# Optimization experiments

Measured on AMD Instinct MI355X. Metric: run time of the kernel, lower is better.

## Reference

```python
import jax, jax.numpy as jnp
import numpy as np

B, HID = 32768, 128
NU = 0.49                 # poisson_ratio default
LAM_PHYS, LAM_EL = 0.1, 0.05
EPS = 1e-7


def setup_inputs() -> dict:
    key = jax.random.key(0)
    ks = jax.random.split(key, 8)
    def w(k, shape, fan_in):
        return jax.random.normal(k, shape, jnp.float32) / np.float32(np.sqrt(fan_in))
    return {
        "coords": jax.random.normal(ks[0], (B, 3), jnp.float32),
        "target_labels": jax.random.uniform(ks[1], (B, 1), jnp.float32),
        "target_stiffness": jax.random.uniform(ks[2], (B, 1), jnp.float32) * 10.0,
        "W1": w(ks[3], (3, HID), 3), "b1": jnp.zeros((HID,), jnp.float32),
        "W2": w(ks[4], (HID, HID), HID), "b2": jnp.zeros((HID,), jnp.float32),
        "Wp": w(ks[5], (HID, 1), HID), "bp": jnp.zeros((1,), jnp.float32),
        "Ws": w(ks[6], (HID, 1), HID), "bs": jnp.zeros((1,), jnp.float32),
        "Wd": w(ks[7], (HID, 3), HID), "bd": jnp.zeros((3,), jnp.float32),
    }


def reference(coords, target_labels, target_stiffness,
              W1, b1, W2, b2, Wp, bp, Ws, bs, Wd, bd):
    def feats(x):  # x: (...,3) -> (...,HID)
        h = jnp.tanh(x @ W1 + b1)
        return jnp.tanh(h @ W2 + b2)

    h = feats(coords)                                   # (B,HID)
    prediction = jax.nn.sigmoid(h @ Wp + bp)            # (B,1)
    stiffness = jax.nn.softplus(h @ Ws + bs)            # (B,1) Young's modulus E

    # displacement field u(x): R^3 -> R^3, pointwise
    def disp_fn(x):  # (3,) -> (3,)
        return feats(x) @ Wd + bd

    # Per-point Hessian H[b,i,j,k] = d2 u_i / dx_j dx_k  (B,3,3,3)
    Hm = jax.vmap(jax.jacfwd(jax.jacfwd(disp_fn)))(coords)
    laplacian = jnp.einsum('bijj->bi', Hm)              # (B,3) lap(u_i)
    grad_div = jnp.einsum('biik->bk', Hm)               # (B,3) grad(div u)

    # Lame parameters from E (matches torch code incl. nu_denom clamp)
    mu = stiffness / (2.0 * (1.0 + NU))
    nu_denom = max(1.0 - 2.0 * NU, 1e-5)
    lmbda = stiffness * NU / ((1.0 + NU) * nu_denom)
    residual = mu * laplacian + (lmbda + mu) * grad_div  # (B,3)
    phys_loss = jnp.mean(jnp.sum(residual ** 2, axis=-1))

    # BCE on clamped prediction/labels
    p = jnp.clip(prediction, EPS, 1.0 - EPS)
    t = jnp.clip(target_labels, 0.0, 1.0)
    bce = -jnp.mean(t * jnp.log(p) + (1.0 - t) * jnp.log(1.0 - p))
    data_loss = bce + 0.5 * jnp.mean((stiffness - target_stiffness) ** 2)

    elastic_loss = jnp.mean(jax.nn.relu(-stiffness) + jax.nn.relu(stiffness - 15.0))

    total = data_loss + LAM_PHYS * phys_loss + LAM_EL * elastic_loss
    raw_losses = jnp.stack([data_loss, phys_loss, elastic_loss])
    return total, raw_losses
```

## Files before the change

### kernel.cpp

```cpp
#include <hip/hip_runtime.h>
#include <math.h>

#define HIDN 128
#define NPTS 32768
#define PTS_PER_BLK 16
#define NBLK (NPTS / PTS_PER_BLK)

#define MU_COEF 0.33557046979865773f
#define LM_COEF 16.442953020134228f

typedef float f32x4  __attribute__((ext_vector_type(4)));
typedef short bf16x8 __attribute__((ext_vector_type(8)));


__device__ __forceinline__ unsigned short f2bf(float f) {
    unsigned u = __builtin_bit_cast(unsigned, f);
    u += 0x7fffu + ((u >> 16) & 1u);
    return (unsigned short)(u >> 16);
}

__device__ __forceinline__ float tanh_fast(float x) {
    float e = __builtin_amdgcn_exp2f(x * 2.885390081777927f);
    return 1.0f - 2.0f * __builtin_amdgcn_rcpf(e + 1.0f);
}

__global__ void prep_kernel(const float* __restrict__ W1,
                            const float* __restrict__ b1,
                            const float* __restrict__ W2,
                            float* __restrict__ ws)
{
    float* accum = ws;
    float* tab   = ws + 128;
    unsigned short* W2bf = (unsigned short*)(ws + 2048);
    int tid = blockIdx.x * blockDim.x + threadIdx.x;
    if (tid < 8) accum[tid] = 0.0f;
    if (tid < HIDN) {
        float w0 = W1[0 * HIDN + tid];
        float w1 = W1[1 * HIDN + tid];
        float w2 = W1[2 * HIDN + tid];
        float* t = tab + tid * 12;
        t[0] = w0; t[1] = w1; t[2] = w2; t[3] = b1[tid];
        t[4] = w0 * w0; t[5] = w0 * w1; t[6] = w0 * w2;
        t[7] = w1 * w1; t[8] = w1 * w2; t[9] = w2 * w2;
        t[10] = 0.0f; t[11] = 0.0f;
    }
    for (int i = tid; i < HIDN * HIDN; i += gridDim.x * blockDim.x) {
        int m = i >> 7, h = i & 127;
        W2bf[m * HIDN + h] = f2bf(W2[h * HIDN + m]);
    }
}

__global__ __launch_bounds__(256, 3) void pinn_main(
    const float* __restrict__ coords,
    const float* __restrict__ labels,
    const float* __restrict__ tstiff,
    const float* __restrict__ b2,
    const float* __restrict__ Wp, const float* __restrict__ bp,
    const float* __restrict__ Wsv, const float* __restrict__ bs,
    const float* __restrict__ Wd,
    const float* __restrict__ ws_ro,
    float* __restrict__ accum)
{
    const float* tab = ws_ro + 128;
    const unsigned short* W2bf = (const unsigned short*)(ws_ro + 2048);

    __shared__ __align__(16) char smem[43584];
    unsigned short* A  = (unsigned short*)smem;
    float*          red  = (float*)smem;
    float*          red2 = (float*)(smem + 43520);

    const int tid  = threadIdx.x;
    const int wave = __builtin_amdgcn_readfirstlane(tid >> 6);
    const int lane = tid & 63;
    const int blk  = blockIdx.x;

    {
        const int b  = tid & 15;
        const int hc = tid >> 4;
        const int h0 = hc * 8;
        const int gb = blk * PTS_PER_BLK + b;
        const float x0 = coords[gb * 3 + 0];
        const float x1 = coords[gb * 3 + 1];
        const float x2 = coords[gb * 3 + 2];
        unsigned pk[10][4];
#pragma unroll
        for (int i = 0; i < 8; ++i) {
            const float* t = tab + (h0 + i) * 12;
            float z = fmaf(x0, t[0], fmaf(x1, t[1], fmaf(x2, t[2], t[3])));
            float a  = tanh_fast(z);
            float g  = fmaf(-a, a, 1.0f);
            float ag = a * g;
            float c[10];
            c[0] = a;
            c[1] = g * t[0]; c[2] = g * t[1]; c[3] = g * t[2];
            c[4] = ag * t[4]; c[5] = ag * t[5]; c[6] = ag * t[6];
            c[7] = ag * t[7]; c[8] = ag * t[8]; c[9] = ag * t[9];
#pragma unroll
            for (int ch = 0; ch < 10; ++ch) {
                unsigned v = f2bf(c[ch]);
                if ((i & 1) == 0) pk[ch][i >> 1] = v;
                else              pk[ch][i >> 1] |= v << 16;
            }
        }
#pragma unroll
        for (int ch = 0; ch < 10; ++ch) {
            uint4* dst = (uint4*)(A + ch * (16 * 136) + b * 136 + h0);
            *dst = make_uint4(pk[ch][0], pk[ch][1], pk[ch][2], pk[ch][3]);
        }
    }
    __syncthreads();

    const int l = lane & 15;
    const int q = lane >> 4;

    f32x4 acc[10][2] = {};
#pragma unroll
    for (int ks = 0; ks < 4; ++ks) {
        const int hk = ks * 32 + q * 8;
        bf16x8 bfr[2];
#pragma unroll
        for (int mt = 0; mt < 2; ++mt) {
            const int m = wave * 32 + mt * 16 + l;
            bfr[mt] = *(const bf16x8*)(W2bf + m * HIDN + hk);
        }
#pragma unroll
        for (int ch = 0; ch < 10; ++ch) {
            bf16x8 afr = *(const bf16x8*)(A + ch * (16 * 136) + l * 136 + hk);
            acc[ch][0] = __builtin_amdgcn_mfma_f32_16x16x32_bf16(afr, bfr[0], acc[ch][0], 0, 0, 0);
            acc[ch][1] = __builtin_amdgcn_mfma_f32_16x16x32_bf16(afr, bfr[1], acc[ch][1], 0, 0, 0);
        }
    }

    float sum[4][8] = {};
#pragma unroll
    for (int mt = 0; mt < 2; ++mt) {
        const int m = wave * 32 + mt * 16 + l;
        const float wd0 = Wd[m * 3 + 0];
        const float wd1 = Wd[m * 3 + 1];
        const float wd2 = Wd[m * 3 + 2];
        const float wp  = Wp[m];
        const float wsv = Wsv[m];
        const float b2v = b2[m];
#pragma unroll
        for (int r = 0; r < 4; ++r) {
            const float z2 = acc[0][mt][r] + b2v;
            const float a2 = tanh_fast(z2);
            const float g2 = fmaf(-a2, a2, 1.0f);
            const float d2 = -2.0f * a2 * g2;
            const float t0 = acc[1][mt][r], t1 = acc[2][mt][r], t2 = acc[3][mt][r];
            const float q00 = acc[4][mt][r], q01 = acc[5][mt][r], q02 = acc[6][mt][r];
            const float q11 = acc[7][mt][r], q12 = acc[8][mt][r], q22 = acc[9][mt][r];
            const float qtr = q00 + q11 + q22;
            const float tt  = t0 * t0 + t1 * t1 + t2 * t2;
            const float Lm  = fmaf(-2.0f * g2, qtr, d2 * tt);
            const float wt  = wd0 * t0 + wd1 * t1 + wd2 * t2;
            const float m2g2 = -2.0f * g2;
            const float dwt  = d2 * wt;
            const float r0 = wd0 * q00 + wd1 * q01 + wd2 * q02;
            const float r1 = wd0 * q01 + wd1 * q11 + wd2 * q12;
            const float r2 = wd0 * q02 + wd1 * q12 + wd2 * q22;
            sum[r][0] += wp  * a2;
            sum[r][1] += wsv * a2;
            sum[r][2] += wd0 * Lm;
            sum[r][3] += wd1 * Lm;
            sum[r][4] += wd2 * Lm;
            sum[r][5] += m2g2 * r0 + dwt * t0;
            sum[r][6] += m2g2 * r1 + dwt * t1;
            sum[r][7] += m2g2 * r2 + dwt * t2;
        }
    }
    __syncthreads();

#pragma unroll
    for (int r = 0; r < 4; ++r) {
        const int b = q * 4 + r;
        const int slot = wave * 16 + l;
        float4* dst = (float4*)(red + (b * 64 + slot) * 8);
        dst[0] = make_float4(sum[r][0], sum[r][1], sum[r][2], sum[r][3]);
        dst[1] = make_float4(sum[r][4], sum[r][5], sum[r][6], sum[r][7]);
    }
    __syncthreads();

    {
        const int b  = tid >> 4;
        const int l2 = tid & 15;
        float v[8] = {};
#pragma unroll
        for (int w = 0; w < 4; ++w) {
            const float4* src = (const float4*)(red + (b * 64 + w * 16 + l2) * 8);
            float4 p0 = src[0], p1 = src[1];
            v[0] += p0.x; v[1] += p0.y; v[2] += p0.z; v[3] += p0.w;
            v[4] += p1.x; v[5] += p1.y; v[6] += p1.z; v[7] += p1.w;
        }
#pragma unroll
        for (int k = 0; k < 8; ++k) {
            v[k] += __shfl_xor(v[k], 1);
            v[k] += __shfl_xor(v[k], 2);
            v[k] += __shfl_xor(v[k], 4);
            v[k] += __shfl_xor(v[k], 8);
        }
        float bce_t = 0.f, sq_t = 0.f, phys_t = 0.f, el_t = 0.f;
        if (l2 == 0) {
            const int gb = blk * PTS_PER_BLK + b;
            const float fzp = v[0] + bp[0];
            const float fzs = v[1] + bs[0];
            float pred = 1.0f / (1.0f + expf(-fzp));
            pred = fminf(fmaxf(pred, 1e-7f), 1.0f - 1e-7f);
            const float E = fmaxf(fzs, 0.0f) + log1pf(expf(-fabsf(fzs)));
            const float mu = E * MU_COEF;
            const float cc = E * LM_COEF + mu;
            const float rr0 = mu * v[2] + cc * v[5];
            const float rr1 = mu * v[3] + cc * v[6];
            const float rr2 = mu * v[4] + cc * v[7];
            phys_t = rr0 * rr0 + rr1 * rr1 + rr2 * rr2;
            float tl = labels[gb];
            tl = fminf(fmaxf(tl, 0.0f), 1.0f);
            bce_t = -(tl * logf(pred) + (1.0f - tl) * logf(1.0f - pred));
            const float dsv = E - tstiff[gb];
            sq_t = dsv * dsv;
            el_t = fmaxf(-E, 0.0f) + fmaxf(E - 15.0f, 0.0f);
        }
#pragma unroll
        for (int m = 16; m < 64; m <<= 1) {
            bce_t  += __shfl_xor(bce_t, m);
            sq_t   += __shfl_xor(sq_t, m);
            phys_t += __shfl_xor(phys_t, m);
            el_t   += __shfl_xor(el_t, m);
        }
        if (lane == 0) {
            red2[wave * 4 + 0] = bce_t;
            red2[wave * 4 + 1] = sq_t;
            red2[wave * 4 + 2] = phys_t;
            red2[wave * 4 + 3] = el_t;
        }
    }
    __syncthreads();
    if (tid < 4) {
        float s = red2[0 * 4 + tid] + red2[1 * 4 + tid] + red2[2 * 4 + tid] + red2[3 * 4 + tid];
        atomicAdd(accum + tid, s);
    }
}

__global__ void finalize_kernel(const float* __restrict__ accum,
                                float* __restrict__ out)
{
    if (threadIdx.x == 0 && blockIdx.x == 0) {
        const float invB = 1.0f / (float)NPTS;
        const float bce  = accum[0] * invB;
        const float data = bce + 0.5f * accum[1] * invB;
        const float phys = accum[2] * invB;
        const float el   = accum[3] * invB;
        out[0] = data + 0.1f * phys + 0.05f * el;
        out[1] = data;
        out[2] = phys;
        out[3] = el;
    }
}

extern "C" void kernel_launch(void* const* d_in, const int* in_sizes, int n_in,
                              void* d_out, int out_size, void* d_ws, size_t ws_size,
                              hipStream_t stream)
{
    const float* coords = (const float*)d_in[0];
    const float* labels = (const float*)d_in[1];
    const float* tstiff = (const float*)d_in[2];
    const float* W1  = (const float*)d_in[3];
    const float* b1  = (const float*)d_in[4];
    const float* W2  = (const float*)d_in[5];
    const float* b2  = (const float*)d_in[6];
    const float* Wp  = (const float*)d_in[7];
    const float* bp  = (const float*)d_in[8];
    const float* Wsv = (const float*)d_in[9];
    const float* bs  = (const float*)d_in[10];
    const float* Wd  = (const float*)d_in[11];

    float* ws  = (float*)d_ws;
    float* out = (float*)d_out;

    prep_kernel<<<64, 256, 0, stream>>>(W1, b1, W2, ws);
    pinn_main<<<NBLK, 256, 0, stream>>>(coords, labels, tstiff, b2,
                                        Wp, bp, Wsv, bs, Wd, ws, ws);
    finalize_kernel<<<1, 64, 0, stream>>>(ws, out);
}
```

Measured before the change: 116.4 us.

## Swizzle LDS layout, swap MFMA operands, and simplify per-block reduction

The first-layer features now go into a row-major LDS tile with an XOR swizzle instead of padded rows, and W1/b1 are read with vector loads in place of a precomputed table. Packing uses the hardware v_cvt_pk_bf16_f32 instruction. The MFMA operands are swapped so each lane's accumulators belong to a single point, which lets the per-point reduction use cross-lane shuffles plus one small LDS pass and drops one barrier. Per-hidden-unit output weights are packed into a vectorized table. The changes target LDS bank conflicts, conversion cost and reduction overhead, at the price of depending on inline asm and a swizzle indexing scheme.

```diff
diff --git a/kernel.cpp b/kernel.cpp
--- a/kernel.cpp
+++ b/kernel.cpp
@@ -12,41 +12,42 @@
 typedef float f32x4  __attribute__((ext_vector_type(4)));
 typedef short bf16x8 __attribute__((ext_vector_type(8)));
 
-
 __device__ __forceinline__ unsigned short f2bf(float f) {
     unsigned u = __builtin_bit_cast(unsigned, f);
     u += 0x7fffu + ((u >> 16) & 1u);
     return (unsigned short)(u >> 16);
 }
 
+__device__ __forceinline__ unsigned cvtpk2(float lo, float hi) {
+    unsigned r;
+    asm("v_cvt_pk_bf16_f32 %0, %1, %2" : "=v"(r) : "v"(lo), "v"(hi));
+    return r;
+}
+
 __device__ __forceinline__ float tanh_fast(float x) {
     float e = __builtin_amdgcn_exp2f(x * 2.885390081777927f);
     return 1.0f - 2.0f * __builtin_amdgcn_rcpf(e + 1.0f);
 }
 
-__global__ void prep_kernel(const float* __restrict__ W1,
-                            const float* __restrict__ b1,
-                            const float* __restrict__ W2,
+__global__ void prep_kernel(const float* __restrict__ W2,
+                            const float* __restrict__ Wd,
+                            const float* __restrict__ Wp,
+                            const float* __restrict__ Wsv,
+                            const float* __restrict__ b2,
                             float* __restrict__ ws)
 {
-    float* accum = ws;
-    float* tab   = ws + 128;
+    int tid = blockIdx.x * blockDim.x + threadIdx.x;
+    if (tid < 8) ws[tid] = 0.0f;
+    if (tid < HIDN) {
+        float* mt = ws + 64 + tid * 8;
+        mt[0] = Wd[tid * 3 + 0]; mt[1] = Wd[tid * 3 + 1]; mt[2] = Wd[tid * 3 + 2];
+        mt[3] = Wp[tid]; mt[4] = Wsv[tid]; mt[5] = b2[tid];
+        mt[6] = 0.0f; mt[7] = 0.0f;
+    }
     unsigned short* W2bf = (unsigned short*)(ws + 2048);
-    int tid = blockIdx.x * blockDim.x + threadIdx.x;
-    if (tid < 8) accum[tid] = 0.0f;
-    if (tid < HIDN) {
-        float w0 = W1[0 * HIDN + tid];
-        float w1 = W1[1 * HIDN + tid];
-        float w2 = W1[2 * HIDN + tid];
-        float* t = tab + tid * 12;
-        t[0] = w0; t[1] = w1; t[2] = w2; t[3] = b1[tid];
-        t[4] = w0 * w0; t[5] = w0 * w1; t[6] = w0 * w2;
-        t[7] = w1 * w1; t[8] = w1 * w2; t[9] = w2 * w2;
-        t[10] = 0.0f; t[11] = 0.0f;
-    }
     for (int i = tid; i < HIDN * HIDN; i += gridDim.x * blockDim.x) {
-        int m = i >> 7, h = i & 127;
-        W2bf[m * HIDN + h] = f2bf(W2[h * HIDN + m]);
+        int h = i >> 7, m = i & 127;
+        W2bf[m * HIDN + h] = f2bf(W2[i]);
     }
 }
 
@@ -54,20 +55,18 @@
     const float* __restrict__ coords,
     const float* __restrict__ labels,
     const float* __restrict__ tstiff,
-    const float* __restrict__ b2,
-    const float* __restrict__ Wp, const float* __restrict__ bp,
-    const float* __restrict__ Wsv, const float* __restrict__ bs,
-    const float* __restrict__ Wd,
+    const float* __restrict__ W1,
+    const float* __restrict__ b1,
+    const float* __restrict__ bp,
+    const float* __restrict__ bs,
     const float* __restrict__ ws_ro,
     float* __restrict__ accum)
 {
-    const float* tab = ws_ro + 128;
+    const float* mtab = ws_ro + 64;
     const unsigned short* W2bf = (const unsigned short*)(ws_ro + 2048);
 
-    __shared__ __align__(16) char smem[43584];
-    unsigned short* A  = (unsigned short*)smem;
-    float*          red  = (float*)smem;
-    float*          red2 = (float*)(smem + 43520);
+    __shared__ __align__(16) char smem[43008];
+    float* red2 = (float*)(smem + 40960);
 
     const int tid  = threadIdx.x;
     const int wave = __builtin_amdgcn_readfirstlane(tid >> 6);
@@ -75,74 +74,85 @@
     const int blk  = blockIdx.x;
 
     {
-        const int b  = tid & 15;
-        const int hc = tid >> 4;
+        const int b  = tid >> 4;
+        const int hc = tid & 15;
         const int h0 = hc * 8;
         const int gb = blk * PTS_PER_BLK + b;
         const float x0 = coords[gb * 3 + 0];
         const float x1 = coords[gb * 3 + 1];
         const float x2 = coords[gb * 3 + 2];
+        const f32x4 w0lo = *(const f32x4*)(W1 + h0);
+        const f32x4 w0hi = *(const f32x4*)(W1 + h0 + 4);
+        const f32x4 w1lo = *(const f32x4*)(W1 + HIDN + h0);
+        const f32x4 w1hi = *(const f32x4*)(W1 + HIDN + h0 + 4);
+        const f32x4 w2lo = *(const f32x4*)(W1 + 2 * HIDN + h0);
+        const f32x4 w2hi = *(const f32x4*)(W1 + 2 * HIDN + h0 + 4);
+        const f32x4 blo  = *(const f32x4*)(b1 + h0);
+        const f32x4 bhi  = *(const f32x4*)(b1 + h0 + 4);
+
         unsigned pk[10][4];
 #pragma unroll
-        for (int i = 0; i < 8; ++i) {
-            const float* t = tab + (h0 + i) * 12;
-            float z = fmaf(x0, t[0], fmaf(x1, t[1], fmaf(x2, t[2], t[3])));
-            float a  = tanh_fast(z);
-            float g  = fmaf(-a, a, 1.0f);
-            float ag = a * g;
-            float c[10];
-            c[0] = a;
-            c[1] = g * t[0]; c[2] = g * t[1]; c[3] = g * t[2];
-            c[4] = ag * t[4]; c[5] = ag * t[5]; c[6] = ag * t[6];
-            c[7] = ag * t[7]; c[8] = ag * t[8]; c[9] = ag * t[9];
-#pragma unroll
-            for (int ch = 0; ch < 10; ++ch) {
-                unsigned v = f2bf(c[ch]);
-                if ((i & 1) == 0) pk[ch][i >> 1] = v;
-                else              pk[ch][i >> 1] |= v << 16;
+        for (int p = 0; p < 4; ++p) {
+            float ca[2][10];
+#pragma unroll
+            for (int s = 0; s < 2; ++s) {
+                const int i = 2 * p + s;
+                const float wa = (i < 4) ? w0lo[i & 3] : w0hi[i & 3];
+                const float wb = (i < 4) ? w1lo[i & 3] : w1hi[i & 3];
+                const float wc = (i < 4) ? w2lo[i & 3] : w2hi[i & 3];
+                const float bb = (i < 4) ? blo[i & 3]  : bhi[i & 3];
+                const float z  = fmaf(x0, wa, fmaf(x1, wb, fmaf(x2, wc, bb)));
+                const float a  = tanh_fast(z);
+                const float g  = fmaf(-a, a, 1.0f);
+                const float ag = a * g;
+                const float p0 = ag * wa, p1 = ag * wb, p2 = ag * wc;
+                ca[s][0] = a;
+                ca[s][1] = g * wa; ca[s][2] = g * wb; ca[s][3] = g * wc;
+                ca[s][4] = p0 * wa; ca[s][5] = p0 * wb; ca[s][6] = p0 * wc;
+                ca[s][7] = p1 * wb; ca[s][8] = p1 * wc; ca[s][9] = p2 * wc;
             }
-        }
+#pragma unroll
+            for (int ch = 0; ch < 10; ++ch)
+                pk[ch][p] = cvtpk2(ca[0][ch], ca[1][ch]);
+        }
+        const int sw = (h0 * 2) ^ ((b & 7) << 4);
 #pragma unroll
         for (int ch = 0; ch < 10; ++ch) {
-            uint4* dst = (uint4*)(A + ch * (16 * 136) + b * 136 + h0);
-            *dst = make_uint4(pk[ch][0], pk[ch][1], pk[ch][2], pk[ch][3]);
+            *(uint4*)(smem + ch * 4096 + b * 256 + sw) =
+                make_uint4(pk[ch][0], pk[ch][1], pk[ch][2], pk[ch][3]);
         }
     }
     __syncthreads();
 
     const int l = lane & 15;
     const int q = lane >> 4;
+    const int lsw = (l & 7) << 4;
 
     f32x4 acc[10][2] = {};
 #pragma unroll
     for (int ks = 0; ks < 4; ++ks) {
         const int hk = ks * 32 + q * 8;
-        bf16x8 bfr[2];
-#pragma unroll
-        for (int mt = 0; mt < 2; ++mt) {
-            const int m = wave * 32 + mt * 16 + l;
-            bfr[mt] = *(const bf16x8*)(W2bf + m * HIDN + hk);
-        }
+        bf16x8 bfr0 = *(const bf16x8*)(W2bf + (wave * 32 + l) * HIDN + hk);
+        bf16x8 bfr1 = *(const bf16x8*)(W2bf + (wave * 32 + 16 + l) * HIDN + hk);
+        const int coff = (ks * 64 + q * 16) ^ lsw;
 #pragma unroll
         for (int ch = 0; ch < 10; ++ch) {
-            bf16x8 afr = *(const bf16x8*)(A + ch * (16 * 136) + l * 136 + hk);
-            acc[ch][0] = __builtin_amdgcn_mfma_f32_16x16x32_bf16(afr, bfr[0], acc[ch][0], 0, 0, 0);
-            acc[ch][1] = __builtin_amdgcn_mfma_f32_16x16x32_bf16(afr, bfr[1], acc[ch][1], 0, 0, 0);
-        }
-    }
-
-    float sum[4][8] = {};
+            bf16x8 afr = *(const bf16x8*)(smem + ch * 4096 + l * 256 + coff);
+            acc[ch][0] = __builtin_amdgcn_mfma_f32_16x16x32_bf16(bfr0, afr, acc[ch][0], 0, 0, 0);
+            acc[ch][1] = __builtin_amdgcn_mfma_f32_16x16x32_bf16(bfr1, afr, acc[ch][1], 0, 0, 0);
+        }
+    }
+
+    float sum[8] = {0, 0, 0, 0, 0, 0, 0, 0};
 #pragma unroll
     for (int mt = 0; mt < 2; ++mt) {
-        const int m = wave * 32 + mt * 16 + l;
-        const float wd0 = Wd[m * 3 + 0];
-        const float wd1 = Wd[m * 3 + 1];
-        const float wd2 = Wd[m * 3 + 2];
-        const float wp  = Wp[m];
-        const float wsv = Wsv[m];
-        const float b2v = b2[m];
 #pragma unroll
         for (int r = 0; r < 4; ++r) {
+            const int m = wave * 32 + mt * 16 + q * 4 + r;
+            const f32x4 mw0 = *(const f32x4*)(mtab + m * 8);
+            const f32x4 mw1 = *(const f32x4*)(mtab + m * 8 + 4);
+            const float wd0 = mw0[0], wd1 = mw0[1], wd2 = mw0[2], wpv = mw0[3];
+            const float wsv = mw1[0], b2v = mw1[1];
             const float z2 = acc[0][mt][r] + b2v;
             const float a2 = tanh_fast(z2);
             const float g2 = fmaf(-a2, a2, 1.0f);
@@ -152,92 +162,76 @@
             const float q11 = acc[7][mt][r], q12 = acc[8][mt][r], q22 = acc[9][mt][r];
             const float qtr = q00 + q11 + q22;
             const float tt  = t0 * t0 + t1 * t1 + t2 * t2;
-            const float Lm  = fmaf(-2.0f * g2, qtr, d2 * tt);
+            const float m2g2 = -2.0f * g2;
+            const float Lm  = fmaf(m2g2, qtr, d2 * tt);
             const float wt  = wd0 * t0 + wd1 * t1 + wd2 * t2;
-            const float m2g2 = -2.0f * g2;
-            const float dwt  = d2 * wt;
+            const float dwt = d2 * wt;
             const float r0 = wd0 * q00 + wd1 * q01 + wd2 * q02;
             const float r1 = wd0 * q01 + wd1 * q11 + wd2 * q12;
             const float r2 = wd0 * q02 + wd1 * q12 + wd2 * q22;
-            sum[r][0] += wp  * a2;
-            sum[r][1] += wsv * a2;
-            sum[r][2] += wd0 * Lm;
-            sum[r][3] += wd1 * Lm;
-            sum[r][4] += wd2 * Lm;
-            sum[r][5] += m2g2 * r0 + dwt * t0;
-            sum[r][6] += m2g2 * r1 + dwt * t1;
-            sum[r][7] += m2g2 * r2 + dwt * t2;
-        }
+            sum[0] = fmaf(wpv, a2, sum[0]);
+            sum[1] = fmaf(wsv, a2, sum[1]);
+            sum[2] = fmaf(wd0, Lm, sum[2]);
+            sum[3] = fmaf(wd1, Lm, sum[3]);
+            sum[4] = fmaf(wd2, Lm, sum[4]);
+            sum[5] += fmaf(m2g2, r0, dwt * t0);
+            sum[6] += fmaf(m2g2, r1, dwt * t1);
+            sum[7] += fmaf(m2g2, r2, dwt * t2);
+        }
+    }
+
+#pragma unroll
+    for (int k = 0; k < 8; ++k) {
+        sum[k] += __shfl_xor(sum[k], 16);
+        sum[k] += __shfl_xor(sum[k], 32);
+    }
+    if (q == 0) {
+        float4* dst = (float4*)(red2 + (wave * 16 + l) * 8);
+        dst[0] = make_float4(sum[0], sum[1], sum[2], sum[3]);
+        dst[1] = make_float4(sum[4], sum[5], sum[6], sum[7]);
     }
     __syncthreads();
 
-#pragma unroll
-    for (int r = 0; r < 4; ++r) {
-        const int b = q * 4 + r;
-        const int slot = wave * 16 + l;
-        float4* dst = (float4*)(red + (b * 64 + slot) * 8);
-        dst[0] = make_float4(sum[r][0], sum[r][1], sum[r][2], sum[r][3]);
-        dst[1] = make_float4(sum[r][4], sum[r][5], sum[r][6], sum[r][7]);
-    }
-    __syncthreads();
-
-    {
-        const int b  = tid >> 4;
-        const int l2 = tid & 15;
-        float v[8] = {};
+    if (tid < 16) {
+        float v[8] = {0, 0, 0, 0, 0, 0, 0, 0};
 #pragma unroll
         for (int w = 0; w < 4; ++w) {
-            const float4* src = (const float4*)(red + (b * 64 + w * 16 + l2) * 8);
-            float4 p0 = src[0], p1 = src[1];
-            v[0] += p0.x; v[1] += p0.y; v[2] += p0.z; v[3] += p0.w;
-            v[4] += p1.x; v[5] += p1.y; v[6] += p1.z; v[7] += p1.w;
-        }
-#pragma unroll
-        for (int k = 0; k < 8; ++k) {
-            v[k] += __shfl_xor(v[k], 1);
-            v[k] += __shfl_xor(v[k], 2);
-            v[k] += __shfl_xor(v[k], 4);
-            v[k] += __shfl_xor(v[k], 8);
-        }
-        float bce_t = 0.f, sq_t = 0.f, phys_t = 0.f, el_t = 0.f;
-        if (l2 == 0) {
-            const int gb = blk * PTS_PER_BLK + b;
-            const float fzp = v[0] + bp[0];
-            const float fzs = v[1] + bs[0];
-            float pred = 1.0f / (1.0f + expf(-fzp));
-            pred = fminf(fmaxf(pred, 1e-7f), 1.0f - 1e-7f);
-            const float E = fmaxf(fzs, 0.0f) + log1pf(expf(-fabsf(fzs)));
-            const float mu = E * MU_COEF;
-            const float cc = E * LM_COEF + mu;
-            const float rr0 = mu * v[2] + cc * v[5];
-            const float rr1 = mu * v[3] + cc * v[6];
-            const float rr2 = mu * v[4] + cc * v[7];
-            phys_t = rr0 * rr0 + rr1 * rr1 + rr2 * rr2;
-            float tl = labels[gb];
-            tl = fminf(fmaxf(tl, 0.0f), 1.0f);
-            bce_t = -(tl * logf(pred) + (1.0f - tl) * logf(1.0f - pred));
-            const float dsv = E - tstiff[gb];
-            sq_t = dsv * dsv;
-            el_t = fmaxf(-E, 0.0f) + fmaxf(E - 15.0f, 0.0f);
-        }
-#pragma unroll
-        for (int m = 16; m < 64; m <<= 1) {
-            bce_t  += __shfl_xor(bce_t, m);
-            sq_t   += __shfl_xor(sq_t, m);
-            phys_t += __shfl_xor(phys_t, m);
-            el_t   += __shfl_xor(el_t, m);
-        }
-        if (lane == 0) {
-            red2[wave * 4 + 0] = bce_t;
-            red2[wave * 4 + 1] = sq_t;
-            red2[wave * 4 + 2] = phys_t;
-            red2[wave * 4 + 3] = el_t;
-        }
-    }
-    __syncthreads();
-    if (tid < 4) {
-        float s = red2[0 * 4 + tid] + red2[1 * 4 + tid] + red2[2 * 4 + tid] + red2[3 * 4 + tid];
-        atomicAdd(accum + tid, s);
+            const float4* s = (const float4*)(red2 + (w * 16 + tid) * 8);
+            const float4 pa = s[0], pb = s[1];
+            v[0] += pa.x; v[1] += pa.y; v[2] += pa.z; v[3] += pa.w;
+            v[4] += pb.x; v[5] += pb.y; v[6] += pb.z; v[7] += pb.w;
+        }
+        const int gb = blk * PTS_PER_BLK + tid;
+        const float fzp = v[0] + bp[0];
+        const float fzs = v[1] + bs[0];
+        float pred = 1.0f / (1.0f + expf(-fzp));
+        pred = fminf(fmaxf(pred, 1e-7f), 1.0f - 1e-7f);
+        const float E = fmaxf(fzs, 0.0f) + log1pf(expf(-fabsf(fzs)));
+        const float mu = E * MU_COEF;
+        const float cc = E * LM_COEF + mu;
+        const float rr0 = mu * v[2] + cc * v[5];
+        const float rr1 = mu * v[3] + cc * v[6];
+        const float rr2 = mu * v[4] + cc * v[7];
+        float phys_t = rr0 * rr0 + rr1 * rr1 + rr2 * rr2;
+        float tl = labels[gb];
+        tl = fminf(fmaxf(tl, 0.0f), 1.0f);
+        float bce_t = -(tl * logf(pred) + (1.0f - tl) * logf(1.0f - pred));
+        const float dsv = E - tstiff[gb];
+        float sq_t = dsv * dsv;
+        float el_t = fmaxf(-E, 0.0f) + fmaxf(E - 15.0f, 0.0f);
+#pragma unroll
+        for (int mk = 1; mk < 16; mk <<= 1) {
+            bce_t  += __shfl_xor(bce_t, mk);
+            sq_t   += __shfl_xor(sq_t, mk);
+            phys_t += __shfl_xor(phys_t, mk);
+            el_t   += __shfl_xor(el_t, mk);
+        }
+        if (tid == 0) {
+            atomicAdd(accum + 0, bce_t);
+            atomicAdd(accum + 1, sq_t);
+            atomicAdd(accum + 2, phys_t);
+            atomicAdd(accum + 3, el_t);
+        }
     }
 }
 
@@ -277,8 +271,8 @@
     float* ws  = (float*)d_ws;
     float* out = (float*)d_out;
 
-    prep_kernel<<<64, 256, 0, stream>>>(W1, b1, W2, ws);
-    pinn_main<<<NBLK, 256, 0, stream>>>(coords, labels, tstiff, b2,
-                                        Wp, bp, Wsv, bs, Wd, ws, ws);
+    prep_kernel<<<64, 256, 0, stream>>>(W2, Wd, Wp, Wsv, b2, ws);
+    pinn_main<<<NBLK, 256, 0, stream>>>(coords, labels, tstiff, W1, b1,
+                                        bp, bs, ws, ws);
     finalize_kernel<<<1, 64, 0, stream>>>(ws, out);
 }
```

Result: slower. 192.4 us (+65.3%).

## Split pinn_main work across 8 waves per block with 512 threads

Applied to the files above, without the earlier changes.

Doubles the block to 512 threads so each thread builds 4 hidden units of the layer-1 tables and each wave owns one 16-column MFMA tile instead of two. This halves per-thread accumulators and registers and raises the launch-bounds occupancy target, so more waves can hide latency. The cross-wave reduction gains a shuffle step that folds column pairs before the shared-memory stage, keeping the same 64-slot layout. The cost is more waves per block, each with less independent work, and B-fragment loads from W2bf that are no longer shared across two tiles.

```diff
diff --git a/kernel.cpp b/kernel.cpp
--- a/kernel.cpp
+++ b/kernel.cpp
@@ -50,7 +50,7 @@
     }
 }
 
-__global__ __launch_bounds__(256, 3) void pinn_main(
+__global__ __launch_bounds__(512, 4) void pinn_main(
     const float* __restrict__ coords,
     const float* __restrict__ labels,
     const float* __restrict__ tstiff,
@@ -76,15 +76,15 @@
 
     {
         const int b  = tid & 15;
-        const int hc = tid >> 4;
-        const int h0 = hc * 8;
+        const int hb = tid >> 4;
+        const int h0 = hb * 4;
         const int gb = blk * PTS_PER_BLK + b;
         const float x0 = coords[gb * 3 + 0];
         const float x1 = coords[gb * 3 + 1];
         const float x2 = coords[gb * 3 + 2];
-        unsigned pk[10][4];
-#pragma unroll
-        for (int i = 0; i < 8; ++i) {
+        unsigned pk[10][2];
+#pragma unroll
+        for (int i = 0; i < 4; ++i) {
             const float* t = tab + (h0 + i) * 12;
             float z = fmaf(x0, t[0], fmaf(x1, t[1], fmaf(x2, t[2], t[3])));
             float a  = tanh_fast(z);
@@ -104,8 +104,8 @@
         }
 #pragma unroll
         for (int ch = 0; ch < 10; ++ch) {
-            uint4* dst = (uint4*)(A + ch * (16 * 136) + b * 136 + h0);
-            *dst = make_uint4(pk[ch][0], pk[ch][1], pk[ch][2], pk[ch][3]);
+            uint2* dst = (uint2*)(A + ch * (16 * 136) + b * 136 + h0);
+            *dst = make_uint2(pk[ch][0], pk[ch][1]);
         }
     }
     __syncthreads();
@@ -113,28 +113,22 @@
     const int l = lane & 15;
     const int q = lane >> 4;
 
-    f32x4 acc[10][2] = {};
+    f32x4 acc[10] = {};
 #pragma unroll
     for (int ks = 0; ks < 4; ++ks) {
         const int hk = ks * 32 + q * 8;
-        bf16x8 bfr[2];
-#pragma unroll
-        for (int mt = 0; mt < 2; ++mt) {
-            const int m = wave * 32 + mt * 16 + l;
-            bfr[mt] = *(const bf16x8*)(W2bf + m * HIDN + hk);
-        }
+        const int m = wave * 16 + l;
+        bf16x8 bfr = *(const bf16x8*)(W2bf + m * HIDN + hk);
 #pragma unroll
         for (int ch = 0; ch < 10; ++ch) {
             bf16x8 afr = *(const bf16x8*)(A + ch * (16 * 136) + l * 136 + hk);
-            acc[ch][0] = __builtin_amdgcn_mfma_f32_16x16x32_bf16(afr, bfr[0], acc[ch][0], 0, 0, 0);
-            acc[ch][1] = __builtin_amdgcn_mfma_f32_16x16x32_bf16(afr, bfr[1], acc[ch][1], 0, 0, 0);
+            acc[ch] = __builtin_amdgcn_mfma_f32_16x16x32_bf16(afr, bfr, acc[ch], 0, 0, 0);
         }
     }
 
     float sum[4][8] = {};
-#pragma unroll
-    for (int mt = 0; mt < 2; ++mt) {
-        const int m = wave * 32 + mt * 16 + l;
+    {
+        const int m = wave * 16 + l;
         const float wd0 = Wd[m * 3 + 0];
         const float wd1 = Wd[m * 3 + 1];
         const float wd2 = Wd[m * 3 + 2];
@@ -143,13 +137,13 @@
         const float b2v = b2[m];
 #pragma unroll
         for (int r = 0; r < 4; ++r) {
-            const float z2 = acc[0][mt][r] + b2v;
+            const float z2 = acc[0][r] + b2v;
             const float a2 = tanh_fast(z2);
             const float g2 = fmaf(-a2, a2, 1.0f);
             const float d2 = -2.0f * a2 * g2;
-            const float t0 = acc[1][mt][r], t1 = acc[2][mt][r], t2 = acc[3][mt][r];
-            const float q00 = acc[4][mt][r], q01 = acc[5][mt][r], q02 = acc[6][mt][r];
-            const float q11 = acc[7][mt][r], q12 = acc[8][mt][r], q22 = acc[9][mt][r];
+            const float t0 = acc[1][r], t1 = acc[2][r], t2 = acc[3][r];
+            const float q00 = acc[4][r], q01 = acc[5][r], q02 = acc[6][r];
+            const float q11 = acc[7][r], q12 = acc[8][r], q22 = acc[9][r];
             const float qtr = q00 + q11 + q22;
             const float tt  = t0 * t0 + t1 * t1 + t2 * t2;
             const float Lm  = fmaf(-2.0f * g2, qtr, d2 * tt);
@@ -169,19 +163,28 @@
             sum[r][7] += m2g2 * r2 + dwt * t2;
         }
     }
-    __syncthreads();
-
-#pragma unroll
-    for (int r = 0; r < 4; ++r) {
-        const int b = q * 4 + r;
-        const int slot = wave * 16 + l;
-        float4* dst = (float4*)(red + (b * 64 + slot) * 8);
-        dst[0] = make_float4(sum[r][0], sum[r][1], sum[r][2], sum[r][3]);
-        dst[1] = make_float4(sum[r][4], sum[r][5], sum[r][6], sum[r][7]);
-    }
-    __syncthreads();
-
-    {
+
+#pragma unroll
+    for (int r = 0; r < 4; ++r)
+#pragma unroll
+        for (int k = 0; k < 8; ++k)
+            sum[r][k] += __shfl_xor(sum[r][k], 8);
+
+    __syncthreads();
+
+    if (l < 8) {
+#pragma unroll
+        for (int r = 0; r < 4; ++r) {
+            const int b = q * 4 + r;
+            const int slot = wave * 8 + l;
+            float4* dst = (float4*)(red + (b * 64 + slot) * 8);
+            dst[0] = make_float4(sum[r][0], sum[r][1], sum[r][2], sum[r][3]);
+            dst[1] = make_float4(sum[r][4], sum[r][5], sum[r][6], sum[r][7]);
+        }
+    }
+    __syncthreads();
+
+    if (tid < 256) {
         const int b  = tid >> 4;
         const int l2 = tid & 15;
         float v[8] = {};
@@ -221,11 +224,11 @@
             el_t = fmaxf(-E, 0.0f) + fmaxf(E - 15.0f, 0.0f);
         }
 #pragma unroll
-        for (int m = 16; m < 64; m <<= 1) {
-            bce_t  += __shfl_xor(bce_t, m);
-            sq_t   += __shfl_xor(sq_t, m);
-            phys_t += __shfl_xor(phys_t, m);
-            el_t   += __shfl_xor(el_t, m);
+        for (int mk = 16; mk < 64; mk <<= 1) {
+            bce_t  += __shfl_xor(bce_t, mk);
+            sq_t   += __shfl_xor(sq_t, mk);
+            phys_t += __shfl_xor(phys_t, mk);
+            el_t   += __shfl_xor(el_t, mk);
         }
         if (lane == 0) {
             red2[wave * 4 + 0] = bce_t;
@@ -278,7 +281,7 @@
     float* out = (float*)d_out;
 
     prep_kernel<<<64, 256, 0, stream>>>(W1, b1, W2, ws);
-    pinn_main<<<NBLK, 256, 0, stream>>>(coords, labels, tstiff, b2,
+    pinn_main<<<NBLK, 512, 0, stream>>>(coords, labels, tstiff, b2,
                                         Wp, bp, Wsv, bs, Wd, ws, ws);
     finalize_kernel<<<1, 64, 0, stream>>>(ws, out);
 }
```

After: 117.9 us. No clear change (+1.3%).

## Process four point tiles per block, keeping W2 fragments in registers

Applied to the files above, without the earlier changes.

Each block now loops over four 16-point tiles instead of one, and the grid shrinks by the same factor. The W2 bf16 B-fragments and the per-column epilogue weights are loaded into registers once and reused for every tile. Loss partials are accumulated across tiles before a single atomic per block. This cuts redundant global weight loads and atomics, but it adds extra barriers per tile, raises register pressure (launch bounds lowered from 3 to 2 blocks per CU), and leaves fewer blocks to hide latency.

```diff
diff --git a/kernel.cpp b/kernel.cpp
--- a/kernel.cpp
+++ b/kernel.cpp
@@ -4,7 +4,8 @@
 #define HIDN 128
 #define NPTS 32768
 #define PTS_PER_BLK 16
-#define NBLK (NPTS / PTS_PER_BLK)
+#define TILES 4
+#define NBLK (NPTS / PTS_PER_BLK / TILES)
 
 #define MU_COEF 0.33557046979865773f
 #define LM_COEF 16.442953020134228f
@@ -50,7 +51,7 @@
     }
 }
 
-__global__ __launch_bounds__(256, 3) void pinn_main(
+__global__ __launch_bounds__(256, 2) void pinn_main(
     const float* __restrict__ coords,
     const float* __restrict__ labels,
     const float* __restrict__ tstiff,
@@ -74,165 +75,189 @@
     const int lane = tid & 63;
     const int blk  = blockIdx.x;
 
-    {
-        const int b  = tid & 15;
-        const int hc = tid >> 4;
-        const int h0 = hc * 8;
-        const int gb = blk * PTS_PER_BLK + b;
-        const float x0 = coords[gb * 3 + 0];
-        const float x1 = coords[gb * 3 + 1];
-        const float x2 = coords[gb * 3 + 2];
-        unsigned pk[10][4];
-#pragma unroll
-        for (int i = 0; i < 8; ++i) {
-            const float* t = tab + (h0 + i) * 12;
-            float z = fmaf(x0, t[0], fmaf(x1, t[1], fmaf(x2, t[2], t[3])));
-            float a  = tanh_fast(z);
-            float g  = fmaf(-a, a, 1.0f);
-            float ag = a * g;
-            float c[10];
-            c[0] = a;
-            c[1] = g * t[0]; c[2] = g * t[1]; c[3] = g * t[2];
-            c[4] = ag * t[4]; c[5] = ag * t[5]; c[6] = ag * t[6];
-            c[7] = ag * t[7]; c[8] = ag * t[8]; c[9] = ag * t[9];
-#pragma unroll
-            for (int ch = 0; ch < 10; ++ch) {
-                unsigned v = f2bf(c[ch]);
-                if ((i & 1) == 0) pk[ch][i >> 1] = v;
-                else              pk[ch][i >> 1] |= v << 16;
-            }
-        }
-#pragma unroll
-        for (int ch = 0; ch < 10; ++ch) {
-            uint4* dst = (uint4*)(A + ch * (16 * 136) + b * 136 + h0);
-            *dst = make_uint4(pk[ch][0], pk[ch][1], pk[ch][2], pk[ch][3]);
-        }
-    }
-    __syncthreads();
-
     const int l = lane & 15;
     const int q = lane >> 4;
 
-    f32x4 acc[10][2] = {};
+    bf16x8 bw[4][2];
 #pragma unroll
     for (int ks = 0; ks < 4; ++ks) {
         const int hk = ks * 32 + q * 8;
-        bf16x8 bfr[2];
-#pragma unroll
-        for (int mt = 0; mt < 2; ++mt) {
-            const int m = wave * 32 + mt * 16 + l;
-            bfr[mt] = *(const bf16x8*)(W2bf + m * HIDN + hk);
-        }
-#pragma unroll
-        for (int ch = 0; ch < 10; ++ch) {
-            bf16x8 afr = *(const bf16x8*)(A + ch * (16 * 136) + l * 136 + hk);
-            acc[ch][0] = __builtin_amdgcn_mfma_f32_16x16x32_bf16(afr, bfr[0], acc[ch][0], 0, 0, 0);
-            acc[ch][1] = __builtin_amdgcn_mfma_f32_16x16x32_bf16(afr, bfr[1], acc[ch][1], 0, 0, 0);
-        }
-    }
-
-    float sum[4][8] = {};
+        bw[ks][0] = *(const bf16x8*)(W2bf + (wave * 32 + l) * HIDN + hk);
+        bw[ks][1] = *(const bf16x8*)(W2bf + (wave * 32 + 16 + l) * HIDN + hk);
+    }
+    float ewd0[2], ewd1[2], ewd2[2], ewp[2], ews[2], eb2[2];
 #pragma unroll
     for (int mt = 0; mt < 2; ++mt) {
         const int m = wave * 32 + mt * 16 + l;
-        const float wd0 = Wd[m * 3 + 0];
-        const float wd1 = Wd[m * 3 + 1];
-        const float wd2 = Wd[m * 3 + 2];
-        const float wp  = Wp[m];
-        const float wsv = Wsv[m];
-        const float b2v = b2[m];
+        ewd0[mt] = Wd[m * 3 + 0];
+        ewd1[mt] = Wd[m * 3 + 1];
+        ewd2[mt] = Wd[m * 3 + 2];
+        ewp[mt]  = Wp[m];
+        ews[mt]  = Wsv[m];
+        eb2[mt]  = b2[m];
+    }
+    const int pb = tid & 15;
+    const int hc = tid >> 4;
+    const int h0 = hc * 8;
+    float cx[TILES][3];
+#pragma unroll
+    for (int t = 0; t < TILES; ++t) {
+        const int gb = (blk * TILES + t) * PTS_PER_BLK + pb;
+        cx[t][0] = coords[gb * 3 + 0];
+        cx[t][1] = coords[gb * 3 + 1];
+        cx[t][2] = coords[gb * 3 + 2];
+    }
+
+    float bce_a = 0.f, sq_a = 0.f, phys_a = 0.f, el_a = 0.f;
+
+    for (int t = 0; t < TILES; ++t) {
+        {
+            const float x0 = cx[t][0];
+            const float x1 = cx[t][1];
+            const float x2 = cx[t][2];
+            unsigned pk[10][4];
+#pragma unroll
+            for (int i = 0; i < 8; ++i) {
+                const float* tt = tab + (h0 + i) * 12;
+                float z = fmaf(x0, tt[0], fmaf(x1, tt[1], fmaf(x2, tt[2], tt[3])));
+                float a  = tanh_fast(z);
+                float g  = fmaf(-a, a, 1.0f);
+                float ag = a * g;
+                float c[10];
+                c[0] = a;
+                c[1] = g * tt[0]; c[2] = g * tt[1]; c[3] = g * tt[2];
+                c[4] = ag * tt[4]; c[5] = ag * tt[5]; c[6] = ag * tt[6];
+                c[7] = ag * tt[7]; c[8] = ag * tt[8]; c[9] = ag * tt[9];
+#pragma unroll
+                for (int ch = 0; ch < 10; ++ch) {
+                    unsigned v = f2bf(c[ch]);
+                    if ((i & 1) == 0) pk[ch][i >> 1] = v;
+                    else              pk[ch][i >> 1] |= v << 16;
+                }
+            }
+#pragma unroll
+            for (int ch = 0; ch < 10; ++ch) {
+                uint4* dst = (uint4*)(A + ch * (16 * 136) + pb * 136 + h0);
+                *dst = make_uint4(pk[ch][0], pk[ch][1], pk[ch][2], pk[ch][3]);
+            }
+        }
+        __syncthreads();
+
+        f32x4 acc[10][2] = {};
+#pragma unroll
+        for (int ks = 0; ks < 4; ++ks) {
+            const int hk = ks * 32 + q * 8;
+#pragma unroll
+            for (int ch = 0; ch < 10; ++ch) {
+                bf16x8 afr = *(const bf16x8*)(A + ch * (16 * 136) + l * 136 + hk);
+                acc[ch][0] = __builtin_amdgcn_mfma_f32_16x16x32_bf16(afr, bw[ks][0], acc[ch][0], 0, 0, 0);
+                acc[ch][1] = __builtin_amdgcn_mfma_f32_16x16x32_bf16(afr, bw[ks][1], acc[ch][1], 0, 0, 0);
+            }
+        }
+
+        float sum[4][8] = {};
+#pragma unroll
+        for (int mt = 0; mt < 2; ++mt) {
+            const float wd0 = ewd0[mt];
+            const float wd1 = ewd1[mt];
+            const float wd2 = ewd2[mt];
+            const float wp  = ewp[mt];
+            const float wsv = ews[mt];
+            const float b2v = eb2[mt];
+#pragma unroll
+            for (int r = 0; r < 4; ++r) {
+                const float z2 = acc[0][mt][r] + b2v;
+                const float a2 = tanh_fast(z2);
+                const float g2 = fmaf(-a2, a2, 1.0f);
+                const float d2 = -2.0f * a2 * g2;
+                const float t0 = acc[1][mt][r], t1 = acc[2][mt][r], t2 = acc[3][mt][r];
+                const float q00 = acc[4][mt][r], q01 = acc[5][mt][r], q02 = acc[6][mt][r];
+                const float q11 = acc[7][mt][r], q12 = acc[8][mt][r], q22 = acc[9][mt][r];
+                const float qtr = q00 + q11 + q22;
+                const float tt  = t0 * t0 + t1 * t1 + t2 * t2;
+                const float Lm  = fmaf(-2.0f * g2, qtr, d2 * tt);
+                const float wt  = wd0 * t0 + wd1 * t1 + wd2 * t2;
+                const float m2g2 = -2.0f * g2;
+                const float dwt  = d2 * wt;
+                const float r0 = wd0 * q00 + wd1 * q01 + wd2 * q02;
+                const float r1 = wd0 * q01 + wd1 * q11 + wd2 * q12;
+                const float r2 = wd0 * q02 + wd1 * q12 + wd2 * q22;
+                sum[r][0] += wp  * a2;
+                sum[r][1] += wsv * a2;
+                sum[r][2] += wd0 * Lm;
+                sum[r][3] += wd1 * Lm;
+                sum[r][4] += wd2 * Lm;
+                sum[r][5] += m2g2 * r0 + dwt * t0;
+                sum[r][6] += m2g2 * r1 + dwt * t1;
+                sum[r][7] += m2g2 * r2 + dwt * t2;
+            }
+        }
+        __syncthreads();
+
 #pragma unroll
         for (int r = 0; r < 4; ++r) {
-            const float z2 = acc[0][mt][r] + b2v;
-            const float a2 = tanh_fast(z2);
-            const float g2 = fmaf(-a2, a2, 1.0f);
-            const float d2 = -2.0f * a2 * g2;
-            const float t0 = acc[1][mt][r], t1 = acc[2][mt][r], t2 = acc[3][mt][r];
-            const float q00 = acc[4][mt][r], q01 = acc[5][mt][r], q02 = acc[6][mt][r];
-            const float q11 = acc[7][mt][r], q12 = acc[8][mt][r], q22 = acc[9][mt][r];
-            const float qtr = q00 + q11 + q22;
-            const float tt  = t0 * t0 + t1 * t1 + t2 * t2;
-            const float Lm  = fmaf(-2.0f * g2, qtr, d2 * tt);
-            const float wt  = wd0 * t0 + wd1 * t1 + wd2 * t2;
-            const float m2g2 = -2.0f * g2;
-            const float dwt  = d2 * wt;
-            const float r0 = wd0 * q00 + wd1 * q01 + wd2 * q02;
-            const float r1 = wd0 * q01 + wd1 * q11 + wd2 * q12;
-            const float r2 = wd0 * q02 + wd1 * q12 + wd2 * q22;
-            sum[r][0] += wp  * a2;
-            sum[r][1] += wsv * a2;
-            sum[r][2] += wd0 * Lm;
-            sum[r][3] += wd1 * Lm;
-            sum[r][4] += wd2 * Lm;
-            sum[r][5] += m2g2 * r0 + dwt * t0;
-            sum[r][6] += m2g2 * r1 + dwt * t1;
-            sum[r][7] += m2g2 * r2 + dwt * t2;
-        }
-    }
-    __syncthreads();
-
-#pragma unroll
-    for (int r = 0; r < 4; ++r) {
-        const int b = q * 4 + r;
-        const int slot = wave * 16 + l;
-        float4* dst = (float4*)(red + (b * 64 + slot) * 8);
-        dst[0] = make_float4(sum[r][0], sum[r][1], sum[r][2], sum[r][3]);
-        dst[1] = make_float4(sum[r][4], sum[r][5], sum[r][6], sum[r][7]);
-    }
-    __syncthreads();
-
-    {
-        const int b  = tid >> 4;
-        const int l2 = tid & 15;
-        float v[8] = {};
-#pragma unroll
-        for (int w = 0; w < 4; ++w) {
-            const float4* src = (const float4*)(red + (b * 64 + w * 16 + l2) * 8);
-            float4 p0 = src[0], p1 = src[1];
-            v[0] += p0.x; v[1] += p0.y; v[2] += p0.z; v[3] += p0.w;
-            v[4] += p1.x; v[5] += p1.y; v[6] += p1.z; v[7] += p1.w;
-        }
-#pragma unroll
-        for (int k = 0; k < 8; ++k) {
-            v[k] += __shfl_xor(v[k], 1);
-            v[k] += __shfl_xor(v[k], 2);
-            v[k] += __shfl_xor(v[k], 4);
-            v[k] += __shfl_xor(v[k], 8);
-        }
-        float bce_t = 0.f, sq_t = 0.f, phys_t = 0.f, el_t = 0.f;
-        if (l2 == 0) {
-            const int gb = blk * PTS_PER_BLK + b;
-            const float fzp = v[0] + bp[0];
-            const float fzs = v[1] + bs[0];
-            float pred = 1.0f / (1.0f + expf(-fzp));
-            pred = fminf(fmaxf(pred, 1e-7f), 1.0f - 1e-7f);
-            const float E = fmaxf(fzs, 0.0f) + log1pf(expf(-fabsf(fzs)));
-            const float mu = E * MU_COEF;
-            const float cc = E * LM_COEF + mu;
-            const float rr0 = mu * v[2] + cc * v[5];
-            const float rr1 = mu * v[3] + cc * v[6];
-            const float rr2 = mu * v[4] + cc * v[7];
-            phys_t = rr0 * rr0 + rr1 * rr1 + rr2 * rr2;
-            float tl = labels[gb];
-            tl = fminf(fmaxf(tl, 0.0f), 1.0f);
-            bce_t = -(tl * logf(pred) + (1.0f - tl) * logf(1.0f - pred));
-            const float dsv = E - tstiff[gb];
-            sq_t = dsv * dsv;
-            el_t = fmaxf(-E, 0.0f) + fmaxf(E - 15.0f, 0.0f);
-        }
-#pragma unroll
-        for (int m = 16; m < 64; m <<= 1) {
-            bce_t  += __shfl_xor(bce_t, m);
-            sq_t   += __shfl_xor(sq_t, m);
-            phys_t += __shfl_xor(phys_t, m);
-            el_t   += __shfl_xor(el_t, m);
-        }
-        if (lane == 0) {
-            red2[wave * 4 + 0] = bce_t;
-            red2[wave * 4 + 1] = sq_t;
-            red2[wave * 4 + 2] = phys_t;
-            red2[wave * 4 + 3] = el_t;
-        }
+            const int b = q * 4 + r;
+            const int slot = wave * 16 + l;
+            float4* dst = (float4*)(red + (b * 64 + slot) * 8);
+            dst[0] = make_float4(sum[r][0], sum[r][1], sum[r][2], sum[r][3]);
+            dst[1] = make_float4(sum[r][4], sum[r][5], sum[r][6], sum[r][7]);
+        }
+        __syncthreads();
+
+        {
+            const int b  = tid >> 4;
+            const int l2 = tid & 15;
+            float v[8] = {};
+#pragma unroll
+            for (int w = 0; w < 4; ++w) {
+                const float4* src = (const float4*)(red + (b * 64 + w * 16 + l2) * 8);
+                float4 p0 = src[0], p1 = src[1];
+                v[0] += p0.x; v[1] += p0.y; v[2] += p0.z; v[3] += p0.w;
+                v[4] += p1.x; v[5] += p1.y; v[6] += p1.z; v[7] += p1.w;
+            }
+#pragma unroll
+            for (int k = 0; k < 8; ++k) {
+                v[k] += __shfl_xor(v[k], 1);
+                v[k] += __shfl_xor(v[k], 2);
+                v[k] += __shfl_xor(v[k], 4);
+                v[k] += __shfl_xor(v[k], 8);
+            }
+            if (l2 == 0) {
+                const int gb = (blk * TILES + t) * PTS_PER_BLK + b;
+                const float fzp = v[0] + bp[0];
+                const float fzs = v[1] + bs[0];
+                float pred = 1.0f / (1.0f + expf(-fzp));
+                pred = fminf(fmaxf(pred, 1e-7f), 1.0f - 1e-7f);
+                const float E = fmaxf(fzs, 0.0f) + log1pf(expf(-fabsf(fzs)));
+                const float mu = E * MU_COEF;
+                const float cc = E * LM_COEF + mu;
+                const float rr0 = mu * v[2] + cc * v[5];
+                const float rr1 = mu * v[3] + cc * v[6];
+                const float rr2 = mu * v[4] + cc * v[7];
+                phys_a += rr0 * rr0 + rr1 * rr1 + rr2 * rr2;
+                float tl = labels[gb];
+                tl = fminf(fmaxf(tl, 0.0f), 1.0f);
+                bce_a += -(tl * logf(pred) + (1.0f - tl) * logf(1.0f - pred));
+                const float dsv = E - tstiff[gb];
+                sq_a += dsv * dsv;
+                el_a += fmaxf(-E, 0.0f) + fmaxf(E - 15.0f, 0.0f);
+            }
+        }
+        __syncthreads();
+    }
+
+#pragma unroll
+    for (int mk = 16; mk < 64; mk <<= 1) {
+        bce_a  += __shfl_xor(bce_a, mk);
+        sq_a   += __shfl_xor(sq_a, mk);
+        phys_a += __shfl_xor(phys_a, mk);
+        el_a   += __shfl_xor(el_a, mk);
+    }
+    if (lane == 0) {
+        red2[wave * 4 + 0] = bce_a;
+        red2[wave * 4 + 1] = sq_a;
+        red2[wave * 4 + 2] = phys_a;
+        red2[wave * 4 + 3] = el_a;
     }
     __syncthreads();
     if (tid < 4) {
```

Measured after the change: 127.1 us. 9.2% more time.
